# Optimization experiments

Measured on AMD Instinct MI355X. Metric: run time of the kernel, lower is better.

## Reference

```python
import jax, jax.numpy as jnp
import numpy as np

N = 150000   # total supergraph nodes (entities+events+chains)
D = 128      # embed_size
H = 4        # attention heads
DH = D // H  # head dim
E = 300000   # edges per layer
L = 4        # layer_specs length
A = 8        # edge attr dim
T = 10       # num_edge_type
TIME_SCALE = 24.0
SLOPE = 0.2  # negative_slope


def setup_inputs() -> dict:
    key = jax.random.key(0)
    ks = jax.random.split(key, 16)
    nrm = lambda k, s, sc=1.0: jax.random.normal(k, s, dtype=jnp.float32) * sc
    return {
        'x': nrm(ks[0], (N, D), 0.1),
        'Wq': nrm(ks[1], (L, D, D), D ** -0.5),
        'Wk': nrm(ks[2], (L, D, D), D ** -0.5),
        'Wv': nrm(ks[3], (L, D, D), D ** -0.5),
        'Wskip': nrm(ks[4], (L, D, D), D ** -0.5),
        'Wa': nrm(ks[5], (L, A, D), 0.1),
        'time_w': nrm(ks[6], (D,)),
        'time_b': nrm(ks[7], (D,), 0.1),
        'dist_w': nrm(ks[8], (D,)),
        'dist_b': nrm(ks[9], (D,), 0.1),
        'type_table': nrm(ks[10], (T, D), 0.1),
        'bn_gamma': jnp.ones((L, D), jnp.float32),
        'bn_beta': jnp.zeros((L, D), jnp.float32),
        'beta': jnp.full((L,), 0.5, jnp.float32),
        'edge_attr': jax.random.uniform(ks[11], (L, E, A), dtype=jnp.float32),
        'edge_dt': jax.random.uniform(ks[12], (L, E), dtype=jnp.float32) * TIME_SCALE,
        'edge_ds': jax.random.uniform(ks[13], (L, E), dtype=jnp.float32) * 10.0,
        'edge_index': jax.random.randint(ks[14], (L, 2, E), 0, N),
        'edge_type': jax.random.randint(ks[15], (L, E), 0, T),
    }


def _layer(x, Wq, Wk, Wv, Wskip, Wa, time_w, time_b, dist_w, dist_b,
           type_table, gamma, bvec, beta, attr, dt, ds, ei, et):
    n = x.shape[0]
    src, dst = ei[0], ei[1]
    # continuous time / distance encoders: cos basis (TimeEncoder / 'time' DistanceEncoder)
    te = jnp.cos((dt / TIME_SCALE)[:, None] * time_w + time_b)   # [E,D]
    de = jnp.cos(ds[:, None] * dist_w + dist_b)                  # [E,D]
    # 'add' edge/time fusion: attr MLP + time + dist + edge-type embeddings
    edge_feat = attr @ Wa + te + de + type_table[et]             # [E,D]
    kv_in = x[src] + edge_feat                                   # gather + fuse
    q = (x @ Wq).reshape(n, H, DH)[dst]                          # [E,H,DH]
    k = (kv_in @ Wk).reshape(-1, H, DH)
    v = (kv_in @ Wv).reshape(-1, H, DH)
    logits = (q * k).sum(-1) * (DH ** -0.5)                      # [E,H]
    logits = jnp.where(logits >= 0, logits, SLOPE * logits)      # leaky_relu(negative_slope)
    # segment softmax over incoming edges of each destination node
    m = jax.ops.segment_max(logits, dst, num_segments=n)
    a = jnp.exp(logits - m[dst])
    denom = jax.ops.segment_sum(a, dst, num_segments=n)
    a = a / denom[dst]
    agg = jax.ops.segment_sum(a[..., None] * v, dst, num_segments=n).reshape(n, D)
    # beta-weighted residual (learn_beta) with skip projection
    out = beta * (x @ Wskip) + (1.0 - beta) * agg
    # BatchNorm1d (training-mode batch stats) + ReLU
    mu = out.mean(0)
    var = out.var(0)
    out = (out - mu) * jax.lax.rsqrt(var + 1e-5) * gamma + bvec
    return jax.nn.relu(out)


def reference(x, Wq, Wk, Wv, Wskip, Wa, time_w, time_b, dist_w, dist_b,
              type_table, bn_gamma, bn_beta, beta, edge_attr, edge_dt,
              edge_ds, edge_index, edge_type):
    for l in range(L):  # entity2event, event2event, event2chain (time filter), chain2chain
        x = _layer(x, Wq[l], Wk[l], Wv[l], Wskip[l], Wa[l],
                   time_w, time_b, dist_w, dist_b, type_table,
                   bn_gamma[l], bn_beta[l], beta[l],
                   edge_attr[l], edge_dt[l], edge_ds[l],
                   edge_index[l], edge_type[l])
    return x
```

## Files before the change

### kernel.cpp

```cpp
#include <hip/hip_runtime.h>

typedef unsigned int u32;
typedef unsigned short u16;
typedef short bf16x8 __attribute__((ext_vector_type(8)));
typedef float f32x4 __attribute__((ext_vector_type(4)));

#define N_NODES 150000
#define E_EDGES 300000
#define L_CNT   151552

__device__ __forceinline__ float b2f(u16 h){ return __uint_as_float(((u32)h) << 16); }
__device__ __forceinline__ u16 f2bf(float f){
  u32 u = __float_as_uint(f);
  return (u16)((u + 0x7fffu + ((u >> 16) & 1u)) >> 16);
}

__device__ __forceinline__ f32x4 mfma16(bf16x8 a, bf16x8 b, f32x4 c){
  return __builtin_amdgcn_mfma_f32_16x16x32_bf16(a, b, c, 0, 0, 0);
}

__device__ __forceinline__ int opsw(int r, int k){ return (r * 128 + k) ^ ((r & 7) << 3); }
__device__ __forceinline__ int csw(int r, int n){ return (r * 128 + n) ^ (((r >> 2) & 3) << 3); }

__global__ __launch_bounds__(256)
void k_wt(const float* __restrict__ Wq, const float* __restrict__ Wk,
          const float* __restrict__ Wv, const float* __restrict__ Ws,
          u16* __restrict__ Wt)
{
  const int m = blockIdx.x;
  const float* src = (m < 4 ? Wq : m < 8 ? Wk : m < 12 ? Wv : Ws)
                     + (size_t)(m & 3) * 16384;
  u16* dst = Wt + (size_t)m * 16384;
  const int t = threadIdx.x;
  for (int i = 0; i < 16; ++i) {
    int idx = i * 256 + t;
    int n = idx >> 5;
    int k4 = (idx & 31) << 2;
    ushort4 o;
    o.x = f2bf(src[(k4 + 0) * 128 + n]);
    o.y = f2bf(src[(k4 + 1) * 128 + n]);
    o.z = f2bf(src[(k4 + 2) * 128 + n]);
    o.w = f2bf(src[(k4 + 3) * 128 + n]);
    *(ushort4*)(dst + n * 128 + k4) = o;
  }
}


__device__ __forceinline__ void acc_zero(f32x4 (&acc)[2][8])
{
  #pragma unroll
  for (int a = 0; a < 2; ++a)
    #pragma unroll
    for (int b = 0; b < 8; ++b) {
      acc[a][b][0] = 0.f; acc[a][b][1] = 0.f;
      acc[a][b][2] = 0.f; acc[a][b][3] = 0.f;
    }
}

__device__ __forceinline__ void acc_to_lds(u16* Cs, f32x4 (&acc)[2][8], int w, int lane)
{
  const int lr = lane & 15;
  const int g4 = (lane >> 4) << 2;
  #pragma unroll
  for (int mt = 0; mt < 2; ++mt)
    #pragma unroll
    for (int nt = 0; nt < 8; ++nt)
      #pragma unroll
      for (int j = 0; j < 4; ++j)
        Cs[csw(w * 32 + mt * 16 + g4 + j, nt * 16 + lr)] = f2bf(acc[mt][nt][j]);
}

__device__ __forceinline__ void lds_to_global(const u16* Cs, u16* __restrict__ G,
                                              int base, int nr, int t)
{
  #pragma unroll
  for (int i = 0; i < 8; ++i) {
    int cid = i * 256 + t;
    int r = cid >> 4, n8 = (cid & 15) << 3;
    if (r < nr) {
      uint4 v = *(const uint4*)(Cs + csw(r, n8));
      *(uint4*)(G + (size_t)(base + r) * 128 + n8) = v;
    }
  }
}


__global__ __launch_bounds__(256)
void k_hist(const int* __restrict__ eidx, int* __restrict__ counts)
{
  const int l = blockIdx.y;
  const int e = blockIdx.x * 256 + threadIdx.x;
  if (e < E_EDGES) {
    int dst = eidx[(size_t)l * 2 * E_EDGES + E_EDGES + e];
    atomicAdd(&counts[(size_t)l * L_CNT + dst], 1);
  }
}

__global__ __launch_bounds__(256)
void k_scan1(const int* __restrict__ counts, int* __restrict__ rowptr,
             int* __restrict__ bsum)
{
  __shared__ int sh[256];
  const int b = blockIdx.x, l = blockIdx.y;
  const int t = threadIdx.x;
  const int* c = counts + (size_t)l * L_CNT + b * 2048;
  int* rp = rowptr + (size_t)l * L_CNT + b * 2048;
  int v[8]; int s = 0;
  #pragma unroll
  for (int j = 0; j < 8; ++j) { v[j] = c[t * 8 + j]; s += v[j]; }
  sh[t] = s; __syncthreads();
  for (int off = 1; off < 256; off <<= 1) {
    int x = (t >= off) ? sh[t - off] : 0;
    __syncthreads();
    sh[t] += x;
    __syncthreads();
  }
  int excl = (t == 0) ? 0 : sh[t - 1];
  if (t == 255) bsum[l * 128 + b] = sh[255];
  int run = excl;
  #pragma unroll
  for (int j = 0; j < 8; ++j) { rp[t * 8 + j] = run; run += v[j]; }
}

__global__ __launch_bounds__(128)
void k_scan2(int* __restrict__ bsum)
{
  __shared__ int sh[128];
  const int l = blockIdx.x, t = threadIdx.x;
  int v = (t < 74) ? bsum[l * 128 + t] : 0;
  sh[t] = v; __syncthreads();
  for (int off = 1; off < 128; off <<= 1) {
    int x = (t >= off) ? sh[t - off] : 0;
    __syncthreads();
    sh[t] += x;
    __syncthreads();
  }
  int excl = (t == 0) ? 0 : sh[t - 1];
  if (t < 74) bsum[l * 128 + t] = excl;
}

__global__ __launch_bounds__(256)
void k_scan3(int* __restrict__ rowptr, int* __restrict__ tmp,
             const int* __restrict__ bsum)
{
  const int l = blockIdx.y;
  const int q = blockIdx.x * 256 + threadIdx.x;
  int v = rowptr[(size_t)l * L_CNT + q] + bsum[l * 128 + (q >> 11)];
  rowptr[(size_t)l * L_CNT + q] = v;
  tmp[(size_t)l * L_CNT + q] = v;
}

__global__ __launch_bounds__(256)
void k_scatter(const int* __restrict__ eidx, int* __restrict__ tmp,
               int* __restrict__ sorted)
{
  const int l = blockIdx.y;
  const int e = blockIdx.x * 256 + threadIdx.x;
  if (e < E_EDGES) {
    int dst = eidx[(size_t)l * 2 * E_EDGES + E_EDGES + e];
    int pos = atomicAdd(&tmp[(size_t)l * L_CNT + dst], 1);
    sorted[(size_t)l * E_EDGES + pos] = e;
  }
}


template<int XF32>
__global__ __launch_bounds__(256)
void gemm_qs(const void* __restrict__ xg, const u16* __restrict__ WtQ,
             const u16* __restrict__ WtS, u16* __restrict__ Qo,
             u16* __restrict__ So)
{
  __shared__ __align__(16) u16 As[16384];
  const int t = threadIdx.x;
  const int w = t >> 6, lane = t & 63;
  const int lr = lane & 15, hi = lane >> 4;
  const int row0 = blockIdx.x * 128;
  const int g = t >> 5, c4 = (t & 31) << 2;
  int nr = N_NODES - row0; if (nr > 128) nr = 128;

  #pragma unroll
  for (int i = 0; i < 16; ++i) {
    int r = i * 8 + g;
    ushort4 o = make_ushort4(0, 0, 0, 0);
    if (r < nr) {
      if (XF32) {
        float4 v = *(const float4*)((const float*)xg + (size_t)(row0 + r) * 128 + c4);
        o.x = f2bf(v.x); o.y = f2bf(v.y); o.z = f2bf(v.z); o.w = f2bf(v.w);
      } else {
        o = *(const ushort4*)((const u16*)xg + (size_t)(row0 + r) * 128 + c4);
      }
    }
    *(ushort4*)(As + opsw(r, c4)) = o;
  }
  __syncthreads();

  f32x4 qacc[2][8], sacc[2][8];
  acc_zero(qacc); acc_zero(sacc);
  #pragma unroll
  for (int ks = 0; ks < 4; ++ks) {
    const int kb = ks * 32 + hi * 8;
    bf16x8 a0 = *(const bf16x8*)(As + opsw(w * 32 + lr, kb));
    bf16x8 a1 = *(const bf16x8*)(As + opsw(w * 32 + 16 + lr, kb));
    #pragma unroll
    for (int nb = 0; nb < 8; ++nb) {
      bf16x8 bq = *(const bf16x8*)(WtQ + (nb * 16 + lr) * 128 + kb);
      bf16x8 bs = *(const bf16x8*)(WtS + (nb * 16 + lr) * 128 + kb);
      qacc[0][nb] = mfma16(a0, bq, qacc[0][nb]);
      qacc[1][nb] = mfma16(a1, bq, qacc[1][nb]);
      sacc[0][nb] = mfma16(a0, bs, sacc[0][nb]);
      sacc[1][nb] = mfma16(a1, bs, sacc[1][nb]);
    }
  }
  __syncthreads();
  acc_to_lds(As, qacc, w, lane);
  __syncthreads();
  lds_to_global(As, Qo, row0, nr, t);
  __syncthreads();
  acc_to_lds(As, sacc, w, lane);
  __syncthreads();
  lds_to_global(As, So, row0, nr, t);
}


template<int XF32>
__global__ __launch_bounds__(256)
void edge_pass(const void* __restrict__ xg, const u16* __restrict__ WtK,
               const u16* __restrict__ WtV, const float* __restrict__ Wa,
               const float* __restrict__ tw, const float* __restrict__ tb,
               const float* __restrict__ dw, const float* __restrict__ db,
               const float* __restrict__ ttab, const float* __restrict__ attr,
               const float* __restrict__ dt, const float* __restrict__ dsv,
               const int* __restrict__ srcA, const int* __restrict__ dstA,
               const int* __restrict__ etA, const int* __restrict__ sortedE,
               const u16* __restrict__ Qb, float* __restrict__ logits,
               u16* __restrict__ Vs)
{
  __shared__ __align__(16) u16 As[16384];
  __shared__ int dstSh[128];
  const int t = threadIdx.x;
  const int w = t >> 6, lane = t & 63;
  const int lr = lane & 15, hi = lane >> 4;
  const int e0 = blockIdx.x * 128;
  const int ne = min(128, E_EDGES - e0);
  const int g = t >> 5, c4 = (t & 31) << 2;

  float4 tw4 = *(const float4*)(tw + c4);
  float4 tb4 = *(const float4*)(tb + c4);
  float4 dw4 = *(const float4*)(dw + c4);
  float4 db4 = *(const float4*)(db + c4);
  float4 wa4[8];
  #pragma unroll
  for (int a = 0; a < 8; ++a) wa4[a] = *(const float4*)(Wa + a * 128 + c4);

  #pragma unroll
  for (int i = 0; i < 16; ++i) {
    int r = i * 8 + g;
    ushort4 o = make_ushort4(0, 0, 0, 0);
    if (r < ne) {
      int eid = sortedE[e0 + r];
      if ((t & 31) == 0) dstSh[r] = dstA[eid];
      int et = etA[eid];
      float dtn = dt[eid] * (1.0f / 24.0f);
      float dss = dsv[eid];
      float4 tt4 = *(const float4*)(ttab + et * 128 + c4);
      float f0 = __cosf(fmaf(dtn, tw4.x, tb4.x)) + __cosf(fmaf(dss, dw4.x, db4.x)) + tt4.x;
      float f1 = __cosf(fmaf(dtn, tw4.y, tb4.y)) + __cosf(fmaf(dss, dw4.y, db4.y)) + tt4.y;
      float f2 = __cosf(fmaf(dtn, tw4.z, tb4.z)) + __cosf(fmaf(dss, dw4.z, db4.z)) + tt4.z;
      float f3 = __cosf(fmaf(dtn, tw4.w, tb4.w)) + __cosf(fmaf(dss, dw4.w, db4.w)) + tt4.w;
      const float* ap = attr + (size_t)eid * 8;
      #pragma unroll
      for (int a = 0; a < 8; ++a) {
        float aa = ap[a];
        f0 = fmaf(aa, wa4[a].x, f0);
        f1 = fmaf(aa, wa4[a].y, f1);
        f2 = fmaf(aa, wa4[a].z, f2);
        f3 = fmaf(aa, wa4[a].w, f3);
      }
      int src = srcA[eid];
      float x0, x1, x2, x3;
      if (XF32) {
        float4 xr = *(const float4*)((const float*)xg + (size_t)src * 128 + c4);
        x0 = xr.x; x1 = xr.y; x2 = xr.z; x3 = xr.w;
      } else {
        ushort4 xr = *(const ushort4*)((const u16*)xg + (size_t)src * 128 + c4);
        x0 = b2f(xr.x); x1 = b2f(xr.y); x2 = b2f(xr.z); x3 = b2f(xr.w);
      }
      o.x = f2bf(x0 + f0);
      o.y = f2bf(x1 + f1);
      o.z = f2bf(x2 + f2);
      o.w = f2bf(x3 + f3);
    } else {
      if ((t & 31) == 0) dstSh[r] = 0;
    }
    *(ushort4*)(As + opsw(r, c4)) = o;
  }
  __syncthreads();

  f32x4 kacc[2][8];
  acc_zero(kacc);
  #pragma unroll
  for (int ks = 0; ks < 4; ++ks) {
    const int kb = ks * 32 + hi * 8;
    bf16x8 ef0 = *(const bf16x8*)(As + opsw(w * 32 + lr, kb));
    bf16x8 ef1 = *(const bf16x8*)(As + opsw(w * 32 + 16 + lr, kb));
    #pragma unroll
    for (int nb = 0; nb < 8; ++nb) {
      bf16x8 af = *(const bf16x8*)(WtK + (nb * 16 + lr) * 128 + kb);
      kacc[0][nb] = mfma16(af, ef0, kacc[0][nb]);
      kacc[1][nb] = mfma16(af, ef1, kacc[1][nb]);
    }
  }

  #pragma unroll
  for (int eb = 0; eb < 2; ++eb) {
    int el = w * 32 + eb * 16 + lr;
    int dstn = dstSh[el];
    float hs[4] = {0.f, 0.f, 0.f, 0.f};
    #pragma unroll
    for (int nb = 0; nb < 8; ++nb) {
      ushort4 q = *(const ushort4*)(Qb + (size_t)dstn * 128 + nb * 16 + hi * 4);
      hs[nb >> 1] += b2f(q.x) * kacc[eb][nb][0] + b2f(q.y) * kacc[eb][nb][1]
                   + b2f(q.z) * kacc[eb][nb][2] + b2f(q.w) * kacc[eb][nb][3];
    }
    #pragma unroll
    for (int h = 0; h < 4; ++h) {
      hs[h] += __shfl_xor(hs[h], 16, 64);
      hs[h] += __shfl_xor(hs[h], 32, 64);
      hs[h] *= 0.17677669529663687f;
      hs[h] = (hs[h] >= 0.f) ? hs[h] : 0.2f * hs[h];
    }
    if (lane < 16 && el < ne)
      *(float4*)(logits + (size_t)(e0 + el) * 4) = make_float4(hs[0], hs[1], hs[2], hs[3]);
  }

  f32x4 vacc[2][8];
  acc_zero(vacc);
  #pragma unroll
  for (int ks = 0; ks < 4; ++ks) {
    const int kb = ks * 32 + hi * 8;
    bf16x8 af0 = *(const bf16x8*)(As + opsw(w * 32 + lr, kb));
    bf16x8 af1 = *(const bf16x8*)(As + opsw(w * 32 + 16 + lr, kb));
    #pragma unroll
    for (int nb = 0; nb < 8; ++nb) {
      bf16x8 bf = *(const bf16x8*)(WtV + (nb * 16 + lr) * 128 + kb);
      vacc[0][nb] = mfma16(af0, bf, vacc[0][nb]);
      vacc[1][nb] = mfma16(af1, bf, vacc[1][nb]);
    }
  }
  __syncthreads();
  acc_to_lds(As, vacc, w, lane);
  __syncthreads();
  lds_to_global(As, Vs, e0, ne, t);
}

__global__ __launch_bounds__(256)
void node_agg(const u16* __restrict__ Vs, const float* __restrict__ logits,
              const int* __restrict__ rowptr, const u16* __restrict__ S,
              const float* __restrict__ betaP, float* __restrict__ pre,
              float* __restrict__ colsum, float* __restrict__ colsumsq)
{
  __shared__ float red[1024];
  const int t = threadIdx.x;
  const int g = t >> 5;
  const int lane = t & 31;
  const int d0 = lane * 4;
  const int h = lane >> 3;
  const float beta = *betaP;
  const float omb = 1.f - beta;
  float s4[4] = {0.f, 0.f, 0.f, 0.f};
  float q4[4] = {0.f, 0.f, 0.f, 0.f};
  for (int rep = 0; rep < 16; ++rep) {
    int n = blockIdx.x * 128 + rep * 8 + g;
    if (n < N_NODES) {
      int rs = rowptr[n], re = rowptr[n + 1];
      float m = -1e30f;
      for (int i = rs; i < re; ++i)
        m = fmaxf(m, logits[(size_t)i * 4 + h]);
      float den = 0.f;
      float a0 = 0.f, a1 = 0.f, a2 = 0.f, a3 = 0.f;
      for (int i = rs; i < re; ++i) {
        float wgt = __expf(logits[(size_t)i * 4 + h] - m);
        den += wgt;
        ushort4 v = *(const ushort4*)(Vs + (size_t)i * 128 + d0);
        a0 = fmaf(wgt, b2f(v.x), a0);
        a1 = fmaf(wgt, b2f(v.y), a1);
        a2 = fmaf(wgt, b2f(v.z), a2);
        a3 = fmaf(wgt, b2f(v.w), a3);
      }
      float inv = (den > 0.f) ? (omb / den) : 0.f;
      ushort4 sv = *(const ushort4*)(S + (size_t)n * 128 + d0);
      float p0 = fmaf(beta, b2f(sv.x), a0 * inv);
      float p1 = fmaf(beta, b2f(sv.y), a1 * inv);
      float p2 = fmaf(beta, b2f(sv.z), a2 * inv);
      float p3 = fmaf(beta, b2f(sv.w), a3 * inv);
      *(float4*)(pre + (size_t)n * 128 + d0) = make_float4(p0, p1, p2, p3);
      s4[0] += p0; s4[1] += p1; s4[2] += p2; s4[3] += p3;
      q4[0] += p0 * p0; q4[1] += p1 * p1; q4[2] += p2 * p2; q4[3] += p3 * p3;
    }
  }
  *(float4*)(&red[g * 128 + d0]) = make_float4(s4[0], s4[1], s4[2], s4[3]);
  __syncthreads();
  if (t < 128) {
    float tot = 0.f;
    #pragma unroll
    for (int gg = 0; gg < 8; ++gg) tot += red[gg * 128 + t];
    atomicAdd(&colsum[t], tot);
  }
  __syncthreads();
  *(float4*)(&red[g * 128 + d0]) = make_float4(q4[0], q4[1], q4[2], q4[3]);
  __syncthreads();
  if (t < 128) {
    float tot = 0.f;
    #pragma unroll
    for (int gg = 0; gg < 8; ++gg) tot += red[gg * 128 + t];
    atomicAdd(&colsumsq[t], tot);
  }
}

template<int LAST>
__global__ __launch_bounds__(256)
void bn_apply(const float* __restrict__ pre, const float* __restrict__ colsum,
              const float* __restrict__ colsumsq, const float* __restrict__ gamma,
              const float* __restrict__ bvec, u16* __restrict__ outbf,
              float* __restrict__ outf)
{
  const int idx = blockIdx.x * 256 + threadIdx.x;
  const int n = idx >> 5;
  const int d0 = (idx & 31) * 4;
  const float invN = 1.f / 150000.f;
  float4 p = *(const float4*)(pre + (size_t)n * 128 + d0);
  float4 cs = *(const float4*)(colsum + d0);
  float4 cq = *(const float4*)(colsumsq + d0);
  float4 gm = *(const float4*)(gamma + d0);
  float4 bv = *(const float4*)(bvec + d0);
  float mu, var, y;
  mu = cs.x * invN; var = cq.x * invN - mu * mu;
  y = (p.x - mu) * rsqrtf(var + 1e-5f) * gm.x + bv.x; p.x = fmaxf(y, 0.f);
  mu = cs.y * invN; var = cq.y * invN - mu * mu;
  y = (p.y - mu) * rsqrtf(var + 1e-5f) * gm.y + bv.y; p.y = fmaxf(y, 0.f);
  mu = cs.z * invN; var = cq.z * invN - mu * mu;
  y = (p.z - mu) * rsqrtf(var + 1e-5f) * gm.z + bv.z; p.z = fmaxf(y, 0.f);
  mu = cs.w * invN; var = cq.w * invN - mu * mu;
  y = (p.w - mu) * rsqrtf(var + 1e-5f) * gm.w + bv.w; p.w = fmaxf(y, 0.f);
  if (LAST) {
    *(float4*)(outf + (size_t)n * 128 + d0) = p;
  } else {
    ushort4 o;
    o.x = f2bf(p.x); o.y = f2bf(p.y); o.z = f2bf(p.z); o.w = f2bf(p.w);
    *(ushort4*)(outbf + (size_t)n * 128 + d0) = o;
  }
}

extern "C" void kernel_launch(void* const* d_in, const int* in_sizes, int n_in,
                              void* d_out, int out_size, void* d_ws, size_t ws_size,
                              hipStream_t stream)
{
  const float* x0    = (const float*)d_in[0];
  const float* Wq    = (const float*)d_in[1];
  const float* Wk    = (const float*)d_in[2];
  const float* Wv    = (const float*)d_in[3];
  const float* Wsk   = (const float*)d_in[4];
  const float* Wa    = (const float*)d_in[5];
  const float* tw    = (const float*)d_in[6];
  const float* tb    = (const float*)d_in[7];
  const float* dw    = (const float*)d_in[8];
  const float* db    = (const float*)d_in[9];
  const float* ttab  = (const float*)d_in[10];
  const float* gam   = (const float*)d_in[11];
  const float* bet   = (const float*)d_in[12];
  const float* betaP = (const float*)d_in[13];
  const float* attr  = (const float*)d_in[14];
  const float* dt    = (const float*)d_in[15];
  const float* dsv   = (const float*)d_in[16];
  const int*   eidx  = (const int*)d_in[17];
  const int*   etyp  = (const int*)d_in[18];

  char* p = (char*)d_ws;
  u16* xbf  = (u16*)p;       p += 38400000;
  u16* Q    = (u16*)p;       p += 38400000;
  u16* S    = (u16*)p;       p += 38400000;
  u16* Vs   = (u16*)p;       p += 76800000;
  float* logits = (float*)p; p += 4800000;
  int* rowptr = (int*)p;     p += 4 * L_CNT * 4;
  int* tmp    = (int*)p;     p += 4 * L_CNT * 4;
  int* sorted = (int*)p;     p += 4 * E_EDGES * 4;
  int* bsum   = (int*)p;     p += 4 * 128 * 4;
  float* colsum   = (float*)p; p += 512;
  float* colsumsq = (float*)p; p += 512;
  u16* Wt = (u16*)p;         p += 16 * 16384 * 2;

  float* pre = (float*)d_out;

  k_wt<<<16, 256, 0, stream>>>(Wq, Wk, Wv, Wsk, Wt);
  hipMemsetAsync(tmp, 0, 4 * L_CNT * 4, stream);
  k_hist<<<dim3(1172, 4), 256, 0, stream>>>(eidx, tmp);
  k_scan1<<<dim3(74, 4), 256, 0, stream>>>(tmp, rowptr, bsum);
  k_scan2<<<4, 128, 0, stream>>>(bsum);
  k_scan3<<<dim3(592, 4), 256, 0, stream>>>(rowptr, tmp, bsum);
  k_scatter<<<dim3(1172, 4), 256, 0, stream>>>(eidx, tmp, sorted);

  for (int l = 0; l < 4; ++l) {
    const int* srcA = eidx + (size_t)l * 600000;
    const int* dstA = srcA + 300000;
    const int* sortedE = sorted + (size_t)l * E_EDGES;
    const int* rpl = rowptr + (size_t)l * L_CNT;
    const u16* WtQl = Wt + (size_t)l * 16384;
    const u16* WtKl = Wt + (size_t)(4 + l) * 16384;
    const u16* WtVl = Wt + (size_t)(8 + l) * 16384;
    const u16* WtSl = Wt + (size_t)(12 + l) * 16384;
    const float* Wal = Wa + (size_t)l * 1024;
    const float* attrl = attr + (size_t)l * 2400000;
    const float* dtl = dt + (size_t)l * 300000;
    const float* dsl = dsv + (size_t)l * 300000;
    const int* etl = etyp + (size_t)l * 300000;

    hipMemsetAsync(colsum, 0, 1024, stream);

    if (l == 0) {
      gemm_qs<1><<<1172, 256, 0, stream>>>((const void*)x0, WtQl, WtSl, Q, S);
      edge_pass<1><<<2344, 256, 0, stream>>>(
          (const void*)x0, WtKl, WtVl, Wal, tw, tb, dw, db, ttab, attrl,
          dtl, dsl, srcA, dstA, etl, sortedE, Q, logits, Vs);
    } else {
      gemm_qs<0><<<1172, 256, 0, stream>>>((const void*)xbf, WtQl, WtSl, Q, S);
      edge_pass<0><<<2344, 256, 0, stream>>>(
          (const void*)xbf, WtKl, WtVl, Wal, tw, tb, dw, db, ttab, attrl,
          dtl, dsl, srcA, dstA, etl, sortedE, Q, logits, Vs);
    }

    node_agg<<<1172, 256, 0, stream>>>(Vs, logits, rpl, S, betaP + l,
                                       pre, colsum, colsumsq);

    if (l < 3)
      bn_apply<0><<<18750, 256, 0, stream>>>(pre, colsum, colsumsq,
                                             gam + (size_t)l * 128,
                                             bet + (size_t)l * 128, xbf, nullptr);
    else
      bn_apply<1><<<18750, 256, 0, stream>>>(pre, colsum, colsumsq,
                                             gam + (size_t)l * 128,
                                             bet + (size_t)l * 128,
                                             nullptr, (float*)d_out);
  }
}
```

Baseline: 1.733 ms.

## Give each wave a private 32-row LDS tile and drop block barriers

The node GEMM and edge-pass kernels now let each of the four waves own an independent 32-row tile with its own LDS slice, instead of sharing a 128-row block tile. This removes every __syncthreads, so a wave can stage, multiply and write back without waiting on the other waves. The goal is to cut barrier stalls and let staging, MFMA and stores from different waves overlap. The cost is slightly more LDS from the padded per-wave slices. Correctness now depends on LDS writes and reads staying ordered within a single wave, with no explicit barrier to enforce it.

Result: no change. 1.707 ms (-1.5%).

```diff
diff --git a/kernel.cpp b/kernel.cpp
--- a/kernel.cpp
+++ b/kernel.cpp
@@ -57,7 +57,7 @@
     }
 }
 
-__device__ __forceinline__ void acc_to_lds(u16* Cs, f32x4 (&acc)[2][8], int w, int lane)
+__device__ __forceinline__ void acc_to_lds(u16* Cs, f32x4 (&acc)[2][8], int lane)
 {
   const int lr = lane & 15;
   const int g4 = (lane >> 4) << 2;
@@ -67,16 +67,16 @@
     for (int nt = 0; nt < 8; ++nt)
       #pragma unroll
       for (int j = 0; j < 4; ++j)
-        Cs[csw(w * 32 + mt * 16 + g4 + j, nt * 16 + lr)] = f2bf(acc[mt][nt][j]);
+        Cs[csw(mt * 16 + g4 + j, nt * 16 + lr)] = f2bf(acc[mt][nt][j]);
 }
 
 __device__ __forceinline__ void lds_to_global(const u16* Cs, u16* __restrict__ G,
-                                              int base, int nr, int t)
+                                              int base, int nr, int lane)
 {
   #pragma unroll
   for (int i = 0; i < 8; ++i) {
-    int cid = i * 256 + t;
-    int r = cid >> 4, n8 = (cid & 15) << 3;
+    int idx = i * 64 + lane;
+    int r = idx >> 4, n8 = (idx & 15) << 3;
     if (r < nr) {
       uint4 v = *(const uint4*)(Cs + csw(r, n8));
       *(uint4*)(G + (size_t)(base + r) * 128 + n8) = v;
@@ -170,17 +170,21 @@
              const u16* __restrict__ WtS, u16* __restrict__ Qo,
              u16* __restrict__ So)
 {
-  __shared__ __align__(16) u16 As[16384];
+  __shared__ __align__(16) u16 AsAll[4][4160];
   const int t = threadIdx.x;
   const int w = t >> 6, lane = t & 63;
+  u16* As = AsAll[w];
   const int lr = lane & 15, hi = lane >> 4;
-  const int row0 = blockIdx.x * 128;
-  const int g = t >> 5, c4 = (t & 31) << 2;
-  int nr = N_NODES - row0; if (nr > 128) nr = 128;
+  const int tile = blockIdx.x * 4 + w;
+  const int row0 = tile * 32;
+  if (row0 >= N_NODES) return;
+  const int nr = min(32, N_NODES - row0);
+  const int g = lane >> 5;
+  const int c4 = (lane & 31) << 2;
 
   #pragma unroll
   for (int i = 0; i < 16; ++i) {
-    int r = i * 8 + g;
+    int r = i * 2 + g;
     ushort4 o = make_ushort4(0, 0, 0, 0);
     if (r < nr) {
       if (XF32) {
@@ -192,15 +196,14 @@
     }
     *(ushort4*)(As + opsw(r, c4)) = o;
   }
-  __syncthreads();
 
   f32x4 qacc[2][8], sacc[2][8];
   acc_zero(qacc); acc_zero(sacc);
   #pragma unroll
   for (int ks = 0; ks < 4; ++ks) {
     const int kb = ks * 32 + hi * 8;
-    bf16x8 a0 = *(const bf16x8*)(As + opsw(w * 32 + lr, kb));
-    bf16x8 a1 = *(const bf16x8*)(As + opsw(w * 32 + 16 + lr, kb));
+    bf16x8 a0 = *(const bf16x8*)(As + opsw(lr, kb));
+    bf16x8 a1 = *(const bf16x8*)(As + opsw(16 + lr, kb));
     #pragma unroll
     for (int nb = 0; nb < 8; ++nb) {
       bf16x8 bq = *(const bf16x8*)(WtQ + (nb * 16 + lr) * 128 + kb);
@@ -211,14 +214,10 @@
       sacc[1][nb] = mfma16(a1, bs, sacc[1][nb]);
     }
   }
-  __syncthreads();
-  acc_to_lds(As, qacc, w, lane);
-  __syncthreads();
-  lds_to_global(As, Qo, row0, nr, t);
-  __syncthreads();
-  acc_to_lds(As, sacc, w, lane);
-  __syncthreads();
-  lds_to_global(As, So, row0, nr, t);
+  acc_to_lds(As, qacc, lane);
+  lds_to_global(As, Qo, row0, nr, lane);
+  acc_to_lds(As, sacc, lane);
+  lds_to_global(As, So, row0, nr, lane);
 }
 
 
@@ -235,14 +234,19 @@
                const u16* __restrict__ Qb, float* __restrict__ logits,
                u16* __restrict__ Vs)
 {
-  __shared__ __align__(16) u16 As[16384];
-  __shared__ int dstSh[128];
+  __shared__ __align__(16) u16 AsAll[4][4160];
+  __shared__ int dstShAll[4][32];
   const int t = threadIdx.x;
   const int w = t >> 6, lane = t & 63;
+  u16* As = AsAll[w];
+  int* dstSh = dstShAll[w];
   const int lr = lane & 15, hi = lane >> 4;
-  const int e0 = blockIdx.x * 128;
-  const int ne = min(128, E_EDGES - e0);
-  const int g = t >> 5, c4 = (t & 31) << 2;
+  const int tile = blockIdx.x * 4 + w;
+  const int e0 = tile * 32;
+  if (e0 >= E_EDGES) return;
+  const int ne = min(32, E_EDGES - e0);
+  const int g = lane >> 5;
+  const int c4 = (lane & 31) << 2;
 
   float4 tw4 = *(const float4*)(tw + c4);
   float4 tb4 = *(const float4*)(tb + c4);
@@ -254,11 +258,11 @@
 
   #pragma unroll
   for (int i = 0; i < 16; ++i) {
-    int r = i * 8 + g;
+    int r = i * 2 + g;
     ushort4 o = make_ushort4(0, 0, 0, 0);
     if (r < ne) {
       int eid = sortedE[e0 + r];
-      if ((t & 31) == 0) dstSh[r] = dstA[eid];
+      if ((lane & 31) == 0) dstSh[r] = dstA[eid];
       int et = etA[eid];
       float dtn = dt[eid] * (1.0f / 24.0f);
       float dss = dsv[eid];
@@ -290,19 +294,18 @@
       o.z = f2bf(x2 + f2);
       o.w = f2bf(x3 + f3);
     } else {
-      if ((t & 31) == 0) dstSh[r] = 0;
+      if ((lane & 31) == 0) dstSh[r] = 0;
     }
     *(ushort4*)(As + opsw(r, c4)) = o;
   }
-  __syncthreads();
 
   f32x4 kacc[2][8];
   acc_zero(kacc);
   #pragma unroll
   for (int ks = 0; ks < 4; ++ks) {
     const int kb = ks * 32 + hi * 8;
-    bf16x8 ef0 = *(const bf16x8*)(As + opsw(w * 32 + lr, kb));
-    bf16x8 ef1 = *(const bf16x8*)(As + opsw(w * 32 + 16 + lr, kb));
+    bf16x8 ef0 = *(const bf16x8*)(As + opsw(lr, kb));
+    bf16x8 ef1 = *(const bf16x8*)(As + opsw(16 + lr, kb));
     #pragma unroll
     for (int nb = 0; nb < 8; ++nb) {
       bf16x8 af = *(const bf16x8*)(WtK + (nb * 16 + lr) * 128 + kb);
@@ -313,7 +316,7 @@
 
   #pragma unroll
   for (int eb = 0; eb < 2; ++eb) {
-    int el = w * 32 + eb * 16 + lr;
+    int el = eb * 16 + lr;
     int dstn = dstSh[el];
     float hs[4] = {0.f, 0.f, 0.f, 0.f};
     #pragma unroll
@@ -338,8 +341,8 @@
   #pragma unroll
   for (int ks = 0; ks < 4; ++ks) {
     const int kb = ks * 32 + hi * 8;
-    bf16x8 af0 = *(const bf16x8*)(As + opsw(w * 32 + lr, kb));
-    bf16x8 af1 = *(const bf16x8*)(As + opsw(w * 32 + 16 + lr, kb));
+    bf16x8 af0 = *(const bf16x8*)(As + opsw(lr, kb));
+    bf16x8 af1 = *(const bf16x8*)(As + opsw(16 + lr, kb));
     #pragma unroll
     for (int nb = 0; nb < 8; ++nb) {
       bf16x8 bf = *(const bf16x8*)(WtV + (nb * 16 + lr) * 128 + kb);
@@ -347,10 +350,8 @@
       vacc[1][nb] = mfma16(af1, bf, vacc[1][nb]);
     }
   }
-  __syncthreads();
-  acc_to_lds(As, vacc, w, lane);
-  __syncthreads();
-  lds_to_global(As, Vs, e0, ne, t);
+  acc_to_lds(As, vacc, lane);
+  lds_to_global(As, Vs, e0, ne, lane);
 }
 
 __global__ __launch_bounds__(256)
```
